# Kernel optimization log

Measured on AMD Instinct MI355X. Metric: run time of the kernel, lower is better.

Reference implementation:

```python
import jax, jax.numpy as jnp
import numpy as np

B, R, A, L, P = 1024, 512, 196, 2, 4  # batch, rnn_size, att_size, num_layers, num_parallels


def setup_inputs() -> dict:
    key = jax.random.key(0)
    ks = jax.random.split(key, 24)
    s = 0.02
    inp = {
        'x': jax.random.normal(ks[0], (B, R), jnp.float32),
        'att': jax.random.normal(ks[1], (B, A, R), jnp.float32),
        'inputs': jax.random.normal(ks[2], (2 * L, B, R), jnp.float32),
        # first attention block
        'Wa2a': jax.random.normal(ks[3], (A, R), jnp.float32) * s,
        'ba2a': jnp.zeros((A,), jnp.float32),
        'Wh2a': jax.random.normal(ks[4], (A, R), jnp.float32) * s,
        'bh2a': jnp.zeros((A,), jnp.float32),
        'Wd2d': jax.random.normal(ks[5], (1, A), jnp.float32) * s,
        'bd2d': jnp.zeros((1,), jnp.float32),
        # second attention block
        'Wa2a1': jax.random.normal(ks[6], (A, R), jnp.float32) * s,
        'ba2a1': jnp.zeros((A,), jnp.float32),
        'Wh2a1': jax.random.normal(ks[7], (A, R), jnp.float32) * s,
        'bh2a1': jnp.zeros((A,), jnp.float32),
        'Wd2d1': jax.random.normal(ks[8], (1, A), jnp.float32) * s,
        'bd2d1': jnp.zeros((1,), jnp.float32),
        # per-parallel LSTM gate linears, stacked over P
        'Wi2h': jax.random.normal(ks[9], (P, 4 * R, R), jnp.float32) * s,
        'bi2h': jnp.zeros((P, 4 * R), jnp.float32),
        'Wh2h': jax.random.normal(ks[10], (P, 4 * R, R), jnp.float32) * s,
        'bh2h': jnp.zeros((P, 4 * R), jnp.float32),
        'Wa2h': jax.random.normal(ks[11], (P, 4 * R, R), jnp.float32) * s,
        'ba2h': jnp.zeros((P, 4 * R), jnp.float32),
    }
    return inp


def _attend(att, h, Wa, ba, Wh, bh, Wd, bd):
    # att: [B, S, R] with S == A (code requires it); h: [B, R]
    av = jnp.einsum('bsr,ar->bsa', att, Wa) + ba            # [B, S, A]
    ah = h @ Wh.T + bh                                      # [B, A]
    # original expands h-projection along the LAST axis (unsqueeze(2).expand)
    dot = jnp.tanh(av + ah[:, :, None])                     # [B, S, A]
    score = jnp.einsum('bsa,a->bs', dot, Wd[0]) + bd[0]     # [B, S]
    w = jax.nn.softmax(score, axis=-1)
    return jnp.einsum('bsr,bs->br', att, w)                 # [B, R]


def reference(x, att, inputs, Wa2a, ba2a, Wh2a, bh2a, Wd2d, bd2d,
              Wa2a1, ba2a1, Wh2a1, bh2a1, Wd2d1, bd2d1,
              Wi2h, bi2h, Wh2h, bh2h, Wa2h, ba2h):
    R_ = x.shape[-1]
    L_ = inputs.shape[0] // 2
    outputs = []
    for i in range(L_):
        prev_c = inputs[2 * i]
        prev_h = inputs[2 * i + 1]
        xt = x if i == 0 else x + outputs[-1]
        att_res = _attend(att, prev_h, Wa2a, ba2a, Wh2a, bh2a, Wd2d, bd2d)
        # stacked per-parallel gate sums: [P, B, 4R]
        sums = (jnp.einsum('bd,pgd->pbg', xt, Wi2h) + bi2h[:, None, :]
                + jnp.einsum('bd,pgd->pbg', prev_h, Wh2h) + bh2h[:, None, :]
                + jnp.einsum('bd,pgd->pbg', att_res, Wa2h) + ba2h[:, None, :])
        ig = jax.nn.sigmoid(sums[..., :R_])
        fg = jax.nn.sigmoid(sums[..., R_:2 * R_])
        og = jax.nn.sigmoid(sums[..., 2 * R_:3 * R_])
        it = jnp.tanh(sums[..., 3 * R_:])
        nc = fg * prev_c[None] + ig * it                    # [P, B, R]
        next_c = nc.mean(axis=0)
        next_h = (og * jnp.tanh(nc)).mean(axis=0)
        att_res1 = _attend(att, next_h, Wa2a1, ba2a1, Wh2a1, bh2a1, Wd2d1, bd2d1)
        top_h = att_res1 + next_h
        outputs.append(next_c)
        outputs.append(top_h)
    return jnp.stack(outputs)  # [2L, B, R]
```

## Files before the change

kernel.cpp:

```cpp
#include <hip/hip_runtime.h>
#include <math.h>

typedef __attribute__((ext_vector_type(8))) unsigned short ushort8_t;
typedef __attribute__((ext_vector_type(8))) short bf16x8;
typedef __attribute__((ext_vector_type(4))) float f32x4;

namespace {

constexpr int Bn = 1024;
constexpr int Rn = 512;
constexpr int An = 196;
constexpr int Gn = 8192;
constexpr int Kcat = 1536;
constexpr int NP = 224;
constexpr long ROWS = (long)Bn * An;

__device__ __forceinline__ float b2f(unsigned short u) {
  union { unsigned int i; float f; } v; v.i = ((unsigned int)u) << 16; return v.f;
}
__device__ __forceinline__ unsigned short f2b(float f) {
  union { float f; unsigned int i; } v; v.f = f;
  unsigned int r = v.i + 0x7fffu + ((v.i >> 16) & 1u);
  return (unsigned short)(r >> 16);
}
__device__ __forceinline__ float sigmf(float x) {
  return __builtin_amdgcn_rcpf(1.f + __expf(-x));
}
__device__ __forceinline__ float tanhf_fast(float x) {
  const float e = __expf(2.f * x);
  return 1.f - 2.f * __builtin_amdgcn_rcpf(e + 1.f);
}

__global__ __launch_bounds__(256)
void f2b_copy(const float* __restrict__ src, unsigned short* __restrict__ dst, long n)
{
  long i = ((long)blockIdx.x * 256 + threadIdx.x) * 8;
  const long stride = (long)gridDim.x * 256 * 8;
  for (; i + 8 <= n; i += stride) {
    float4 a = *(const float4*)(src + i);
    float4 b = *(const float4*)(src + i + 4);
    ushort8_t o;
    o[0] = f2b(a.x); o[1] = f2b(a.y); o[2] = f2b(a.z); o[3] = f2b(a.w);
    o[4] = f2b(b.x); o[5] = f2b(b.y); o[6] = f2b(b.z); o[7] = f2b(b.w);
    *(ushort8_t*)(dst + i) = o;
  }
}

__global__ __launch_bounds__(256)
void pack_wpad(const float* __restrict__ Wa0, const float* __restrict__ Wa1,
               unsigned short* __restrict__ Wp)
{
  long i = ((long)blockIdx.x * 256 + threadIdx.x) * 8;
  if (i >= 2L * NP * 512) return;
  const int set = (int)(i / (NP * 512));
  const int rem = (int)(i % (NP * 512));
  const int row = rem / 512, k = rem % 512;
  ushort8_t o;
  if (row < An) {
    const float* s = (set ? Wa1 : Wa0) + (long)row * 512 + k;
    float4 a = *(const float4*)s, b = *(const float4*)(s + 4);
    o[0] = f2b(a.x); o[1] = f2b(a.y); o[2] = f2b(a.z); o[3] = f2b(a.w);
    o[4] = f2b(b.x); o[5] = f2b(b.y); o[6] = f2b(b.z); o[7] = f2b(b.w);
  } else {
    o = ushort8_t{0,0,0,0,0,0,0,0};
  }
  *(ushort8_t*)(Wp + i) = o;
}

__global__ __launch_bounds__(256)
void pack_w(const float* __restrict__ Wi, const float* __restrict__ Wh,
            const float* __restrict__ Wa, unsigned short* __restrict__ W2)
{
  long i = ((long)blockIdx.x * 256 + threadIdx.x) * 8;
  if (i >= (long)Gn * Kcat) return;
  const int g = (int)(i / Kcat);
  const int k = (int)(i % Kcat);
  const float* src = (k < 512) ? Wi + (long)g * 512 + k
                   : (k < 1024) ? Wh + (long)g * 512 + (k - 512)
                   : Wa + (long)g * 512 + (k - 1024);
  float4 a = *(const float4*)src;
  float4 b = *(const float4*)(src + 4);
  ushort8_t o;
  o[0] = f2b(a.x); o[1] = f2b(a.y); o[2] = f2b(a.z); o[3] = f2b(a.w);
  o[4] = f2b(b.x); o[5] = f2b(b.y); o[6] = f2b(b.z); o[7] = f2b(b.w);
  *(ushort8_t*)(W2 + i) = o;
}

__global__ __launch_bounds__(256)
void pack_x(const float* __restrict__ xa, const float* __restrict__ xb,
            const float* __restrict__ h, const float* __restrict__ a,
            unsigned short* __restrict__ X2)
{
  long i = ((long)blockIdx.x * 256 + threadIdx.x) * 8;
  if (i >= (long)Bn * Kcat) return;
  const int b = (int)(i / Kcat);
  const int k = (int)(i % Kcat);
  ushort8_t o;
  if (k < 512) {
    const float* s = xa + (long)b * 512 + k;
    float4 v0 = *(const float4*)s, v1 = *(const float4*)(s + 4);
    if (xb) {
      const float* s2 = xb + (long)b * 512 + k;
      float4 w0 = *(const float4*)s2, w1 = *(const float4*)(s2 + 4);
      v0.x += w0.x; v0.y += w0.y; v0.z += w0.z; v0.w += w0.w;
      v1.x += w1.x; v1.y += w1.y; v1.z += w1.z; v1.w += w1.w;
    }
    o[0] = f2b(v0.x); o[1] = f2b(v0.y); o[2] = f2b(v0.z); o[3] = f2b(v0.w);
    o[4] = f2b(v1.x); o[5] = f2b(v1.y); o[6] = f2b(v1.z); o[7] = f2b(v1.w);
  } else {
    const float* s = (k < 1024) ? h + (long)b * 512 + (k - 512)
                                : a + (long)b * 512 + (k - 1024);
    float4 v0 = *(const float4*)s, v1 = *(const float4*)(s + 4);
    o[0] = f2b(v0.x); o[1] = f2b(v0.y); o[2] = f2b(v0.z); o[3] = f2b(v0.w);
    o[4] = f2b(v1.x); o[5] = f2b(v1.y); o[6] = f2b(v1.z); o[7] = f2b(v1.w);
  }
  *(ushort8_t*)(X2 + i) = o;
}

__global__ __launch_bounds__(512)
void av_all(const float* __restrict__ A32,
            unsigned short* __restrict__ att_out,
            const unsigned short* __restrict__ Wcat,
            const float* __restrict__ b0vec, const float* __restrict__ b1vec,
            const float* __restrict__ Wd,
            const float* __restrict__ ah0, const float* __restrict__ ah1,
            float* __restrict__ s0, float* __restrict__ s1,
            unsigned short* __restrict__ av_out)
{
  constexpr int LDP = 40;
  __shared__ unsigned short As[128 * LDP];
  __shared__ unsigned short Bs[448 * LDP];
  __shared__ float wds[NP], bas0[NP], bas1[NP];
  __shared__ float ahAs[128], ahBs[128];
  __shared__ float sbA[128], sbB[128];

  const int tid = threadIdx.x;
  const int lane = tid & 63, wid = tid >> 6;
  const int wr = wid >> 2, wc = wid & 3;
  const int fr = lane & 15, q = lane >> 4, kg = q * 8;
  const long row0 = (long)blockIdx.x * 128;

  if (tid < NP) {
    bas0[tid] = (tid < An) ? b0vec[tid] : 0.f;
    bas1[tid] = (tid < An) ? b1vec[tid] : 0.f;
    wds[tid]  = (tid < An) ? Wd[tid] : 0.f;
  }
  if (tid >= 256 && tid < 384) {
    ahAs[tid - 256] = ah0[row0 + tid - 256];
    ahBs[tid - 256] = ah1[row0 + tid - 256];
  }

  f32x4 acc[4][7] = {};

  const int arow = tid >> 2, akc = (tid & 3) * 8;
  const float* Ap = A32 + (row0 + arow) * 512 + akc;
  unsigned short* Aout = att_out + (row0 + arow) * 512 + akc;
  const bool bload = tid < 448;
  const unsigned short* Bp = Wcat + (long)tid * 512;

  float4 fa0 = *(const float4*)Ap;
  float4 fa1 = *(const float4*)(Ap + 4);
  ushort8_t pb0{}, pb1{}, pb2{}, pb3{};
  if (bload) {
    pb0 = *(const ushort8_t*)(Bp);
    pb1 = *(const ushort8_t*)(Bp + 8);
    pb2 = *(const ushort8_t*)(Bp + 16);
    pb3 = *(const ushort8_t*)(Bp + 24);
  }
  const int swA = arow * LDP + akc;
  const int swB = tid * LDP;

  for (int kt = 0; kt < 512; kt += 32) {
    ushort8_t ua;
    ua[0] = f2b(fa0.x); ua[1] = f2b(fa0.y); ua[2] = f2b(fa0.z); ua[3] = f2b(fa0.w);
    ua[4] = f2b(fa1.x); ua[5] = f2b(fa1.y); ua[6] = f2b(fa1.z); ua[7] = f2b(fa1.w);
    *(ushort8_t*)&As[swA] = ua;
    *(ushort8_t*)(Aout + kt) = ua;
    if (bload) {
      *(ushort8_t*)&Bs[swB] = pb0;
      *(ushort8_t*)&Bs[swB + 8] = pb1;
      *(ushort8_t*)&Bs[swB + 16] = pb2;
      *(ushort8_t*)&Bs[swB + 24] = pb3;
    }
    if (kt + 32 < 512) {
      fa0 = *(const float4*)(Ap + kt + 32);
      fa1 = *(const float4*)(Ap + kt + 36);
      if (bload) {
        pb0 = *(const ushort8_t*)(Bp + kt + 32);
        pb1 = *(const ushort8_t*)(Bp + kt + 40);
        pb2 = *(const ushort8_t*)(Bp + kt + 48);
        pb3 = *(const ushort8_t*)(Bp + kt + 56);
      }
    }
    __syncthreads();
    bf16x8 af[4], bfr[7];
#pragma unroll
    for (int m = 0; m < 4; ++m)
      af[m] = *(const bf16x8*)&As[(wr * 64 + m * 16 + fr) * LDP + kg];
#pragma unroll
    for (int n = 0; n < 7; ++n)
      bfr[n] = *(const bf16x8*)&Bs[(wc * 112 + n * 16 + fr) * LDP + kg];
#pragma unroll
    for (int m = 0; m < 4; ++m)
#pragma unroll
      for (int n = 0; n < 7; ++n)
        acc[m][n] = __builtin_amdgcn_mfma_f32_16x16x32_bf16(af[m], bfr[n], acc[m][n], 0, 0, 0);
    __syncthreads();
  }

  float pA[4][4], pB[4][4];
#pragma unroll
  for (int m = 0; m < 4; ++m)
#pragma unroll
    for (int j = 0; j < 4; ++j) { pA[m][j] = 0.f; pB[m][j] = 0.f; }

  if (wc < 2) {
#pragma unroll
    for (int n = 0; n < 7; ++n) {
      const int col = wc * 112 + n * 16 + fr;
      const float wd = wds[col];
      const float bv = bas0[col];
#pragma unroll
      for (int m = 0; m < 4; ++m) {
#pragma unroll
        for (int j = 0; j < 4; ++j) {
          const int rl = wr * 64 + m * 16 + q * 4 + j;
          const float av = acc[m][n][j] + bv;
          pA[m][j] += wd * tanhf_fast(av + ahAs[rl]);
          pB[m][j] += wd * tanhf_fast(av + ahBs[rl]);
        }
      }
    }
#pragma unroll
    for (int m = 0; m < 4; ++m)
#pragma unroll
      for (int j = 0; j < 4; ++j) {
#pragma unroll
        for (int off = 1; off < 16; off <<= 1) {
          pA[m][j] += __shfl_xor(pA[m][j], off);
          pB[m][j] += __shfl_xor(pB[m][j], off);
        }
      }
  } else {
#pragma unroll
    for (int n = 0; n < 7; ++n) {
      const int col1 = (wc - 2) * 112 + n * 16 + fr;
      if (col1 >= An) continue;
      const float bv = bas1[col1];
#pragma unroll
      for (int m = 0; m < 4; ++m) {
#pragma unroll
        for (int j = 0; j < 4; ++j) {
          const long row = row0 + wr * 64 + m * 16 + q * 4 + j;
          av_out[row * An + col1] = f2b(acc[m][n][j] + bv);
        }
      }
    }
  }
  __syncthreads();
  if (wc == 0 && fr == 0) {
#pragma unroll
    for (int m = 0; m < 4; ++m)
#pragma unroll
      for (int j = 0; j < 4; ++j) {
        const int rl = wr * 64 + m * 16 + q * 4 + j;
        sbA[rl] = pA[m][j]; sbB[rl] = pB[m][j];
      }
  }
  __syncthreads();
  if (wc == 1 && fr == 0) {
#pragma unroll
    for (int m = 0; m < 4; ++m)
#pragma unroll
      for (int j = 0; j < 4; ++j) {
        const int rl = wr * 64 + m * 16 + q * 4 + j;
        sbA[rl] += pA[m][j]; sbB[rl] += pB[m][j];
      }
  }
  __syncthreads();
  if (tid < 128) {
    s0[row0 + tid] = sbA[tid];
    s1[row0 + tid] = sbB[tid];
  }
}

__global__ __launch_bounds__(256)
void gemm_bf(const unsigned short* __restrict__ A, const unsigned short* __restrict__ Bm,
             const float* __restrict__ bias, float* __restrict__ C,
             int N, int K, int ldc)
{
  constexpr int LDP = 40;
  __shared__ unsigned short As[128 * LDP];
  __shared__ unsigned short Bs[128 * LDP];
  const int tid = threadIdx.x;
  const long row0 = (long)blockIdx.y * 128;
  const int col0 = blockIdx.x * 128;
  const int wid = tid >> 6, lane = tid & 63;
  const int wr = wid >> 1, wc = wid & 1;
  const int fr = lane & 15, kg = (lane >> 4) * 8;

  f32x4 acc[4][4] = {};

  const int srow = tid >> 1;
  const int skh = tid & 1;
  const unsigned short* Ap = A + (row0 + srow) * (long)K + skh * 16;
  const int bcol = col0 + srow;
  const unsigned short* Bp = Bm + (long)(bcol < N ? bcol : N - 1) * K + skh * 16;

  ushort8_t a0 = *(const ushort8_t*)(Ap);
  ushort8_t a1 = *(const ushort8_t*)(Ap + 8);
  ushort8_t b0 = *(const ushort8_t*)(Bp);
  ushort8_t b1 = *(const ushort8_t*)(Bp + 8);

  const int sw = srow * LDP + skh * 16;
  for (int kt = 0; kt < K; kt += 32) {
    *(ushort8_t*)&As[sw] = a0;
    *(ushort8_t*)&As[sw + 8] = a1;
    *(ushort8_t*)&Bs[sw] = b0;
    *(ushort8_t*)&Bs[sw + 8] = b1;
    if (kt + 32 < K) {
      a0 = *(const ushort8_t*)(Ap + kt + 32);
      a1 = *(const ushort8_t*)(Ap + kt + 40);
      b0 = *(const ushort8_t*)(Bp + kt + 32);
      b1 = *(const ushort8_t*)(Bp + kt + 40);
    }
    __syncthreads();
    bf16x8 af[4], bfr[4];
#pragma unroll
    for (int m = 0; m < 4; ++m)
      af[m] = *(const bf16x8*)&As[(wr * 64 + m * 16 + fr) * LDP + kg];
#pragma unroll
    for (int n = 0; n < 4; ++n)
      bfr[n] = *(const bf16x8*)&Bs[(wc * 64 + n * 16 + fr) * LDP + kg];
#pragma unroll
    for (int m = 0; m < 4; ++m)
#pragma unroll
      for (int n = 0; n < 4; ++n)
        acc[m][n] = __builtin_amdgcn_mfma_f32_16x16x32_bf16(af[m], bfr[n], acc[m][n], 0, 0, 0);
    __syncthreads();
  }

  const int crow = wr * 64 + (lane >> 4) * 4;
  const int ccol = wc * 64 + fr;
#pragma unroll
  for (int n = 0; n < 4; ++n) {
    const int col = col0 + ccol + n * 16;
    if (col >= N) continue;
    const float bv = bias ? bias[col] : 0.f;
#pragma unroll
    for (int m = 0; m < 4; ++m) {
      const long rb = row0 + crow + m * 16;
#pragma unroll
      for (int j = 0; j < 4; ++j)
        C[(rb + j) * (long)ldc + col] = acc[m][n][j] + bv;
    }
  }
}

__global__ __launch_bounds__(256)
void score1(const unsigned short* __restrict__ av, const float* __restrict__ ah,
            const float* __restrict__ Wd, float* __restrict__ s0)
{
  const int row = blockIdx.x * 4 + (threadIdx.x >> 6);
  const int lane = threadIdx.x & 63;
  const unsigned short* avp = av + (long)row * An;
  const float A0 = ah[row];
  float v0 = 0.f;
  for (int a = lane; a < An; a += 64)
    v0 += Wd[a] * tanhf_fast(b2f(avp[a]) + A0);
#pragma unroll
  for (int o = 32; o; o >>= 1) v0 += __shfl_down(v0, o);
  if (lane == 0) s0[row] = v0;
}

__global__ __launch_bounds__(256)
void softmax_rows(float* __restrict__ sc)
{
  const int b = blockIdx.x;
  const int t = threadIdx.x;
  float x = (t < An) ? sc[(long)b * An + t] : -3.0e38f;
  float m = x;
#pragma unroll
  for (int o = 32; o > 0; o >>= 1) m = fmaxf(m, __shfl_down(m, o));
  __shared__ float red[4];
  __shared__ float bmax, bsumv;
  const int wid = t >> 6;
  if ((t & 63) == 0) red[wid] = m;
  __syncthreads();
  if (t == 0) bmax = fmaxf(fmaxf(red[0], red[1]), fmaxf(red[2], red[3]));
  __syncthreads();
  float e = (t < An) ? __expf(x - bmax) : 0.f;
  float sm = e;
#pragma unroll
  for (int o = 32; o > 0; o >>= 1) sm += __shfl_down(sm, o);
  if ((t & 63) == 0) red[wid] = sm;
  __syncthreads();
  if (t == 0) bsumv = red[0] + red[1] + red[2] + red[3];
  __syncthreads();
  if (t < An) sc[(long)b * An + t] = e / bsumv;
}

template<bool DUAL>
__global__ __launch_bounds__(256)
void wsum2(const unsigned short* __restrict__ att,
           const float* __restrict__ w0, const float* __restrict__ w1,
           const float* __restrict__ add0,
           float* __restrict__ o0, float* __restrict__ o1)
{
  const int half = threadIdx.x >> 7;
  const int b = blockIdx.x * 2 + half;
  const int t = threadIdx.x & 127;
  __shared__ float ws0[2][An], ws1[2][An];
  for (int s = t; s < An; s += 128) {
    ws0[half][s] = w0[(long)b * An + s];
    if (DUAL) ws1[half][s] = w1[(long)b * An + s];
  }
  __syncthreads();
  const unsigned short* ap = att + (long)b * An * Rn + t * 4;
  float a00 = 0, a01 = 0, a02 = 0, a03 = 0;
  float a10 = 0, a11 = 0, a12 = 0, a13 = 0;
  for (int s = 0; s < An; ++s) {
    ushort4 u = *(const ushort4*)(ap + (long)s * Rn);
    const float f0 = b2f(u.x), f1 = b2f(u.y), f2 = b2f(u.z), f3 = b2f(u.w);
    const float v0 = ws0[half][s];
    a00 = fmaf(f0, v0, a00); a01 = fmaf(f1, v0, a01);
    a02 = fmaf(f2, v0, a02); a03 = fmaf(f3, v0, a03);
    if (DUAL) {
      const float v1 = ws1[half][s];
      a10 = fmaf(f0, v1, a10); a11 = fmaf(f1, v1, a11);
      a12 = fmaf(f2, v1, a12); a13 = fmaf(f3, v1, a13);
    }
  }
  const long base = (long)b * Rn + t * 4;
  if (add0) {
    float4 ad = *(const float4*)(add0 + base);
    a00 += ad.x; a01 += ad.y; a02 += ad.z; a03 += ad.w;
  }
  float4 r0 = make_float4(a00, a01, a02, a03);
  *(float4*)(o0 + base) = r0;
  if (DUAL) *(float4*)(o1 + base) = make_float4(a10, a11, a12, a13);
}

__global__ __launch_bounds__(256)
void gates_pw(const float* __restrict__ sums, const float* __restrict__ prev_c,
              float* __restrict__ out_c, float* __restrict__ nh,
              unsigned short* __restrict__ nh_bf)
{
  const int i = blockIdx.x * 256 + threadIdx.x;
  const int b = i >> 9;
  const int r = i & 511;
  const float c = prev_c[i];
  float aC = 0.f, aH = 0.f;
#pragma unroll
  for (int p = 0; p < 4; ++p) {
    const float* sp = sums + (long)b * Gn + p * 2048 + r;
    const float ig = sigmf(sp[0]);
    const float fg = sigmf(sp[512]);
    const float og = sigmf(sp[1024]);
    const float it = tanhf_fast(sp[1536]);
    const float nc = fmaf(fg, c, ig * it);
    aC += nc;
    aH = fmaf(og, tanhf_fast(nc), aH);
  }
  out_c[i] = aC * 0.25f;
  const float hv = aH * 0.25f;
  nh[i] = hv;
  nh_bf[i] = f2b(hv);
}

__global__ __launch_bounds__(256)
void bias3(const float* __restrict__ a, const float* __restrict__ b,
           const float* __restrict__ c, float* __restrict__ o, int n)
{
  const int i = blockIdx.x * 256 + threadIdx.x;
  if (i < n) o[i] = a[i] + b[i] + c[i];
}

}

extern "C" void kernel_launch(void* const* d_in, const int* in_sizes, int n_in,
                              void* d_out, int out_size, void* d_ws, size_t ws_size,
                              hipStream_t stream)
{
  const float* x      = (const float*)d_in[0];
  const float* att    = (const float*)d_in[1];
  const float* inputs = (const float*)d_in[2];
  const float* Wa2a   = (const float*)d_in[3];
  const float* ba2a   = (const float*)d_in[4];
  const float* Wh2a   = (const float*)d_in[5];
  const float* bh2a   = (const float*)d_in[6];
  const float* Wd2d   = (const float*)d_in[7];
  const float* Wa2a1  = (const float*)d_in[9];
  const float* ba2a1  = (const float*)d_in[10];
  const float* Wh2a1  = (const float*)d_in[11];
  const float* bh2a1  = (const float*)d_in[12];
  const float* Wd2d1  = (const float*)d_in[13];
  const float* Wi2h   = (const float*)d_in[15];
  const float* bi2h   = (const float*)d_in[16];
  const float* Wh2h   = (const float*)d_in[17];
  const float* bh2h   = (const float*)d_in[18];
  const float* Wa2h   = (const float*)d_in[19];
  const float* ba2h   = (const float*)d_in[20];
  (void)in_sizes; (void)n_in; (void)out_size; (void)ws_size;

  float* out = (float*)d_out;
  const float* prev_c0 = inputs + 0 * (long)Bn * Rn;
  const float* prev_h0 = inputs + 1 * (long)Bn * Rn;
  const float* prev_c1 = inputs + 2 * (long)Bn * Rn;
  const float* prev_h1 = inputs + 3 * (long)Bn * Rn;

  char* wsp = (char*)d_ws;
  size_t off = 0;
  auto alloc = [&](size_t bytes) -> void* {
    void* p = wsp + off;
    off += (bytes + 1023) & ~(size_t)1023;
    return p;
  };
  unsigned short* att_bf  = (unsigned short*)alloc(ROWS * Rn * 2);
  unsigned short* W2      = (unsigned short*)alloc((size_t)Gn * Kcat * 2);
  unsigned short* Wpad    = (unsigned short*)alloc((size_t)2 * NP * Rn * 2);
  unsigned short* wh2a_bf = (unsigned short*)alloc((size_t)An * Rn * 2);
  unsigned short* wh2a1_bf= (unsigned short*)alloc((size_t)An * Rn * 2);
  unsigned short* h0_bf   = (unsigned short*)alloc((size_t)Bn * Rn * 2);
  unsigned short* h1_bf   = (unsigned short*)alloc((size_t)Bn * Rn * 2);
  unsigned short* nh_bf   = (unsigned short*)alloc((size_t)Bn * Rn * 2);
  unsigned short* X2      = (unsigned short*)alloc((size_t)Bn * Kcat * 2);
  unsigned short* av1_bf  = (unsigned short*)alloc(ROWS * An * 2);
  float* ahA  = (float*)alloc(ROWS * 4);
  float* ahB  = (float*)alloc(ROWS * 4);
  float* ah1  = (float*)alloc(ROWS * 4);
  float* scA  = (float*)alloc(ROWS * 4);
  float* scB  = (float*)alloc(ROWS * 4);
  float* sc1  = (float*)alloc(ROWS * 4);
  float* res0 = (float*)alloc((size_t)Bn * Rn * 4);
  float* res1 = (float*)alloc((size_t)Bn * Rn * 4);
  float* nh   = (float*)alloc((size_t)Bn * Rn * 4);
  float* bsum = (float*)alloc((size_t)Gn * 4);
  float* sums = (float*)alloc((size_t)Bn * Gn * 4);

  const dim3 blk(256);

  pack_wpad<<<dim3(112), blk, 0, stream>>>(Wa2a, Wa2a1, Wpad);
  f2b_copy<<<dim3(49), blk, 0, stream>>>(Wh2a,  wh2a_bf,  (long)An * Rn);
  f2b_copy<<<dim3(49), blk, 0, stream>>>(Wh2a1, wh2a1_bf, (long)An * Rn);
  f2b_copy<<<dim3(256), blk, 0, stream>>>(prev_h0, h0_bf, (long)Bn * Rn);
  f2b_copy<<<dim3(256), blk, 0, stream>>>(prev_h1, h1_bf, (long)Bn * Rn);
  pack_w<<<dim3(6144), blk, 0, stream>>>(Wi2h, Wh2h, Wa2h, W2);
  bias3<<<dim3(Gn / 256), blk, 0, stream>>>(bi2h, bh2h, ba2h, bsum, Gn);

  gemm_bf<<<dim3(2, Bn / 128), blk, 0, stream>>>(h0_bf, wh2a_bf, bh2a, ahA, An, Rn, An);
  gemm_bf<<<dim3(2, Bn / 128), blk, 0, stream>>>(h1_bf, wh2a_bf, bh2a, ahB, An, Rn, An);

  av_all<<<dim3((int)(ROWS / 128)), dim3(512), 0, stream>>>(
      att, att_bf, Wpad, ba2a, ba2a1, Wd2d, ahA, ahB, scA, scB, av1_bf);
  softmax_rows<<<dim3(Bn), blk, 0, stream>>>(scA);
  softmax_rows<<<dim3(Bn), blk, 0, stream>>>(scB);
  wsum2<true><<<dim3(Bn / 2), blk, 0, stream>>>(att_bf, scA, scB, (const float*)nullptr, res0, res1);

  pack_x<<<dim3(768), blk, 0, stream>>>(x, (const float*)nullptr, prev_h0, res0, X2);
  gemm_bf<<<dim3(Gn / 128, Bn / 128), blk, 0, stream>>>(X2, W2, bsum, sums, Gn, Kcat, Gn);
  gates_pw<<<dim3(Bn * Rn / 256), blk, 0, stream>>>(sums, prev_c0, out + 0, nh, nh_bf);

  gemm_bf<<<dim3(2, Bn / 128), blk, 0, stream>>>(nh_bf, wh2a1_bf, bh2a1, ah1, An, Rn, An);
  score1<<<dim3((int)(ROWS / 4)), blk, 0, stream>>>(av1_bf, ah1, Wd2d1, sc1);
  softmax_rows<<<dim3(Bn), blk, 0, stream>>>(sc1);
  wsum2<false><<<dim3(Bn / 2), blk, 0, stream>>>(att_bf, sc1, (const float*)nullptr, nh,
                                                 out + (long)Bn * Rn, (float*)nullptr);

  pack_x<<<dim3(768), blk, 0, stream>>>(x, out + (long)Bn * Rn, prev_h1, res1, X2);
  gemm_bf<<<dim3(Gn / 128, Bn / 128), blk, 0, stream>>>(X2, W2, bsum, sums, Gn, Kcat, Gn);
  gates_pw<<<dim3(Bn * Rn / 256), blk, 0, stream>>>(sums, prev_c1, out + 2 * (long)Bn * Rn, nh, nh_bf);

  gemm_bf<<<dim3(2, Bn / 128), blk, 0, stream>>>(nh_bf, wh2a1_bf, bh2a1, ah1, An, Rn, An);
  score1<<<dim3((int)(ROWS / 4)), blk, 0, stream>>>(av1_bf, ah1, Wd2d1, sc1);
  softmax_rows<<<dim3(Bn), blk, 0, stream>>>(sc1);
  wsum2<false><<<dim3(Bn / 2), blk, 0, stream>>>(att_bf, sc1, (const float*)nullptr, nh,
                                                 out + 3 * (long)Bn * Rn, (float*)nullptr);
}
```

Before: 737.4 us.

## Fuse softmax into weighted sum, add direct-to-LDS gate GEMM, pre-convert att

Removes the separate softmax_rows launches and computes the row softmax inside wsum2 before the weighted sum. Adds a dedicated gate GEMM that uses global_load_lds direct-to-LDS loads and a swizzled block order in place of the generic gemm_bf. The att fp32-to-bf16 conversion moves out of the attention GEMM into a standalone f2b_copy pass. LDS padding grows from 40 to 56. The standalone conversion adds an extra full pass over att, and the new gate GEMM has no padding or double buffering, so LDS bank conflicts and exposed load latency are possible.

```diff
diff --git a/kernel.cpp b/kernel.cpp
--- a/kernel.cpp
+++ b/kernel.cpp
@@ -118,16 +118,15 @@
 }
 
 __global__ __launch_bounds__(512)
-void av_all(const float* __restrict__ A32,
-            unsigned short* __restrict__ att_out,
-            const unsigned short* __restrict__ Wcat,
-            const float* __restrict__ b0vec, const float* __restrict__ b1vec,
-            const float* __restrict__ Wd,
-            const float* __restrict__ ah0, const float* __restrict__ ah1,
-            float* __restrict__ s0, float* __restrict__ s1,
-            unsigned short* __restrict__ av_out)
-{
-  constexpr int LDP = 40;
+void av_both(const unsigned short* __restrict__ A,
+             const unsigned short* __restrict__ Wcat,
+             const float* __restrict__ b0vec, const float* __restrict__ b1vec,
+             const float* __restrict__ Wd,
+             const float* __restrict__ ah0, const float* __restrict__ ah1,
+             float* __restrict__ s0, float* __restrict__ s1,
+             unsigned short* __restrict__ av_out)
+{
+  constexpr int LDP = 56;
   __shared__ unsigned short As[128 * LDP];
   __shared__ unsigned short Bs[448 * LDP];
   __shared__ float wds[NP], bas0[NP], bas1[NP];
@@ -153,13 +152,11 @@
   f32x4 acc[4][7] = {};
 
   const int arow = tid >> 2, akc = (tid & 3) * 8;
-  const float* Ap = A32 + (row0 + arow) * 512 + akc;
-  unsigned short* Aout = att_out + (row0 + arow) * 512 + akc;
+  const unsigned short* Ap = A + (row0 + arow) * 512 + akc;
   const bool bload = tid < 448;
   const unsigned short* Bp = Wcat + (long)tid * 512;
 
-  float4 fa0 = *(const float4*)Ap;
-  float4 fa1 = *(const float4*)(Ap + 4);
+  ushort8_t pa = *(const ushort8_t*)Ap;
   ushort8_t pb0{}, pb1{}, pb2{}, pb3{};
   if (bload) {
     pb0 = *(const ushort8_t*)(Bp);
@@ -171,11 +168,7 @@
   const int swB = tid * LDP;
 
   for (int kt = 0; kt < 512; kt += 32) {
-    ushort8_t ua;
-    ua[0] = f2b(fa0.x); ua[1] = f2b(fa0.y); ua[2] = f2b(fa0.z); ua[3] = f2b(fa0.w);
-    ua[4] = f2b(fa1.x); ua[5] = f2b(fa1.y); ua[6] = f2b(fa1.z); ua[7] = f2b(fa1.w);
-    *(ushort8_t*)&As[swA] = ua;
-    *(ushort8_t*)(Aout + kt) = ua;
+    *(ushort8_t*)&As[swA] = pa;
     if (bload) {
       *(ushort8_t*)&Bs[swB] = pb0;
       *(ushort8_t*)&Bs[swB + 8] = pb1;
@@ -183,8 +176,7 @@
       *(ushort8_t*)&Bs[swB + 24] = pb3;
     }
     if (kt + 32 < 512) {
-      fa0 = *(const float4*)(Ap + kt + 32);
-      fa1 = *(const float4*)(Ap + kt + 36);
+      pa = *(const ushort8_t*)(Ap + kt + 32);
       if (bload) {
         pb0 = *(const ushort8_t*)(Bp + kt + 32);
         pb1 = *(const ushort8_t*)(Bp + kt + 40);
@@ -285,11 +277,78 @@
 }
 
 __global__ __launch_bounds__(256)
+void gemm_gate(const unsigned short* __restrict__ A, const unsigned short* __restrict__ Bm,
+               const float* __restrict__ bias, float* __restrict__ C)
+{
+  __shared__ unsigned short As[128 * 32];
+  __shared__ unsigned short Bs[128 * 32];
+  const int tid = threadIdx.x;
+  const int lane = tid & 63, w = tid >> 6;
+  int bid = blockIdx.x;
+  bid = (bid & 7) * (gridDim.x >> 3) + (bid >> 3);
+  const int bx = bid & 63;
+  const int by = bid >> 6;
+  const long row0 = (long)by * 128;
+  const long col0 = (long)bx * 128;
+  const int wr = w >> 1, wc = w & 1;
+  const int fr = lane & 15, q = lane >> 4;
+  const int srow = lane >> 2, schk = lane & 3;
+
+  f32x4 acc[4][4] = {};
+  const unsigned short* A0 = A + row0 * Kcat + schk * 8;
+  const unsigned short* B0 = Bm + col0 * Kcat + schk * 8;
+
+  for (int kt = 0; kt < Kcat; kt += 32) {
+#pragma unroll
+    for (int i = 0; i < 2; ++i) {
+      const int rr = (w * 2 + i) * 16 + srow;
+      __builtin_amdgcn_global_load_lds(
+          (const __attribute__((address_space(1))) unsigned int*)(A0 + (long)rr * Kcat + kt),
+          (__attribute__((address_space(3))) unsigned int*)(As + (w * 2 + i) * 512),
+          16, 0, 0);
+      __builtin_amdgcn_global_load_lds(
+          (const __attribute__((address_space(1))) unsigned int*)(B0 + (long)rr * Kcat + kt),
+          (__attribute__((address_space(3))) unsigned int*)(Bs + (w * 2 + i) * 512),
+          16, 0, 0);
+    }
+    __syncthreads();
+    bf16x8 af[4], bfr[4];
+#pragma unroll
+    for (int m = 0; m < 4; ++m)
+      af[m] = *(const bf16x8*)&As[(wr * 64 + m * 16 + fr) * 32 + q * 8];
+#pragma unroll
+    for (int n = 0; n < 4; ++n)
+      bfr[n] = *(const bf16x8*)&Bs[(wc * 64 + n * 16 + fr) * 32 + q * 8];
+#pragma unroll
+    for (int m = 0; m < 4; ++m)
+#pragma unroll
+      for (int n = 0; n < 4; ++n)
+        acc[m][n] = __builtin_amdgcn_mfma_f32_16x16x32_bf16(af[m], bfr[n], acc[m][n], 0, 0, 0);
+    __syncthreads();
+  }
+
+  const int crow = wr * 64 + q * 4;
+  const int ccol = wc * 64 + fr;
+#pragma unroll
+  for (int n = 0; n < 4; ++n) {
+    const int col = (int)col0 + ccol + n * 16;
+    const float bv = bias[col];
+#pragma unroll
+    for (int m = 0; m < 4; ++m) {
+      const long rb = row0 + crow + m * 16;
+#pragma unroll
+      for (int j = 0; j < 4; ++j)
+        C[(rb + j) * (long)Gn + col] = acc[m][n][j] + bv;
+    }
+  }
+}
+
+__global__ __launch_bounds__(256)
 void gemm_bf(const unsigned short* __restrict__ A, const unsigned short* __restrict__ Bm,
              const float* __restrict__ bias, float* __restrict__ C,
              int N, int K, int ldc)
 {
-  constexpr int LDP = 40;
+  constexpr int LDP = 56;
   __shared__ unsigned short As[128 * LDP];
   __shared__ unsigned short Bs[128 * LDP];
   const int tid = threadIdx.x;
@@ -373,33 +432,6 @@
   if (lane == 0) s0[row] = v0;
 }
 
-__global__ __launch_bounds__(256)
-void softmax_rows(float* __restrict__ sc)
-{
-  const int b = blockIdx.x;
-  const int t = threadIdx.x;
-  float x = (t < An) ? sc[(long)b * An + t] : -3.0e38f;
-  float m = x;
-#pragma unroll
-  for (int o = 32; o > 0; o >>= 1) m = fmaxf(m, __shfl_down(m, o));
-  __shared__ float red[4];
-  __shared__ float bmax, bsumv;
-  const int wid = t >> 6;
-  if ((t & 63) == 0) red[wid] = m;
-  __syncthreads();
-  if (t == 0) bmax = fmaxf(fmaxf(red[0], red[1]), fmaxf(red[2], red[3]));
-  __syncthreads();
-  float e = (t < An) ? __expf(x - bmax) : 0.f;
-  float sm = e;
-#pragma unroll
-  for (int o = 32; o > 0; o >>= 1) sm += __shfl_down(sm, o);
-  if ((t & 63) == 0) red[wid] = sm;
-  __syncthreads();
-  if (t == 0) bsumv = red[0] + red[1] + red[2] + red[3];
-  __syncthreads();
-  if (t < An) sc[(long)b * An + t] = e / bsumv;
-}
-
 template<bool DUAL>
 __global__ __launch_bounds__(256)
 void wsum2(const unsigned short* __restrict__ att,
@@ -410,12 +442,53 @@
   const int half = threadIdx.x >> 7;
   const int b = blockIdx.x * 2 + half;
   const int t = threadIdx.x & 127;
+  const int wv = t >> 6;
   __shared__ float ws0[2][An], ws1[2][An];
-  for (int s = t; s < An; s += 128) {
-    ws0[half][s] = w0[(long)b * An + s];
-    if (DUAL) ws1[half][s] = w1[(long)b * An + s];
-  }
+  __shared__ float redm[2][2][2], redsum[2][2][2];
+
+  const float r0a = w0[(long)b * An + t];
+  const float r0b = (t + 128 < An) ? w0[(long)b * An + t + 128] : -3.0e38f;
+  float r1a = -3.0e38f, r1b = -3.0e38f;
+  if (DUAL) {
+    r1a = w1[(long)b * An + t];
+    r1b = (t + 128 < An) ? w1[(long)b * An + t + 128] : -3.0e38f;
+  }
+  float m0 = fmaxf(r0a, r0b), m1 = fmaxf(r1a, r1b);
+#pragma unroll
+  for (int o = 32; o; o >>= 1) {
+    m0 = fmaxf(m0, __shfl_xor(m0, o));
+    if (DUAL) m1 = fmaxf(m1, __shfl_xor(m1, o));
+  }
+  if ((t & 63) == 0) { redm[0][half][wv] = m0; if (DUAL) redm[1][half][wv] = m1; }
   __syncthreads();
+  m0 = fmaxf(redm[0][half][0], redm[0][half][1]);
+  if (DUAL) m1 = fmaxf(redm[1][half][0], redm[1][half][1]);
+  const float e0a = __expf(r0a - m0);
+  const float e0b = (t + 128 < An) ? __expf(r0b - m0) : 0.f;
+  float sl0 = e0a + e0b, sl1 = 0.f;
+  float e1a = 0.f, e1b = 0.f;
+  if (DUAL) {
+    e1a = __expf(r1a - m1);
+    e1b = (t + 128 < An) ? __expf(r1b - m1) : 0.f;
+    sl1 = e1a + e1b;
+  }
+#pragma unroll
+  for (int o = 32; o; o >>= 1) {
+    sl0 += __shfl_xor(sl0, o);
+    if (DUAL) sl1 += __shfl_xor(sl1, o);
+  }
+  if ((t & 63) == 0) { redsum[0][half][wv] = sl0; if (DUAL) redsum[1][half][wv] = sl1; }
+  __syncthreads();
+  const float inv0 = __builtin_amdgcn_rcpf(redsum[0][half][0] + redsum[0][half][1]);
+  ws0[half][t] = e0a * inv0;
+  if (t + 128 < An) ws0[half][t + 128] = e0b * inv0;
+  if (DUAL) {
+    const float inv1 = __builtin_amdgcn_rcpf(redsum[1][half][0] + redsum[1][half][1]);
+    ws1[half][t] = e1a * inv1;
+    if (t + 128 < An) ws1[half][t + 128] = e1b * inv1;
+  }
+  __syncthreads();
+
   const unsigned short* ap = att + (long)b * An * Rn + t * 4;
   float a00 = 0, a01 = 0, a02 = 0, a03 = 0;
   float a10 = 0, a11 = 0, a12 = 0, a13 = 0;
@@ -436,8 +509,7 @@
     float4 ad = *(const float4*)(add0 + base);
     a00 += ad.x; a01 += ad.y; a02 += ad.z; a03 += ad.w;
   }
-  float4 r0 = make_float4(a00, a01, a02, a03);
-  *(float4*)(o0 + base) = r0;
+  *(float4*)(o0 + base) = make_float4(a00, a01, a02, a03);
   if (DUAL) *(float4*)(o1 + base) = make_float4(a10, a11, a12, a13);
 }
 
@@ -540,6 +612,7 @@
 
   const dim3 blk(256);
 
+  f2b_copy<<<dim3(50176), blk, 0, stream>>>(att, att_bf, ROWS * Rn);
   pack_wpad<<<dim3(112), blk, 0, stream>>>(Wa2a, Wa2a1, Wpad);
   f2b_copy<<<dim3(49), blk, 0, stream>>>(Wh2a,  wh2a_bf,  (long)An * Rn);
   f2b_copy<<<dim3(49), blk, 0, stream>>>(Wh2a1, wh2a1_bf, (long)An * Rn);
@@ -551,29 +624,25 @@
   gemm_bf<<<dim3(2, Bn / 128), blk, 0, stream>>>(h0_bf, wh2a_bf, bh2a, ahA, An, Rn, An);
   gemm_bf<<<dim3(2, Bn / 128), blk, 0, stream>>>(h1_bf, wh2a_bf, bh2a, ahB, An, Rn, An);
 
-  av_all<<<dim3((int)(ROWS / 128)), dim3(512), 0, stream>>>(
-      att, att_bf, Wpad, ba2a, ba2a1, Wd2d, ahA, ahB, scA, scB, av1_bf);
-  softmax_rows<<<dim3(Bn), blk, 0, stream>>>(scA);
-  softmax_rows<<<dim3(Bn), blk, 0, stream>>>(scB);
+  av_both<<<dim3((int)(ROWS / 128)), dim3(512), 0, stream>>>(
+      att_bf, Wpad, ba2a, ba2a1, Wd2d, ahA, ahB, scA, scB, av1_bf);
   wsum2<true><<<dim3(Bn / 2), blk, 0, stream>>>(att_bf, scA, scB, (const float*)nullptr, res0, res1);
 
   pack_x<<<dim3(768), blk, 0, stream>>>(x, (const float*)nullptr, prev_h0, res0, X2);
-  gemm_bf<<<dim3(Gn / 128, Bn / 128), blk, 0, stream>>>(X2, W2, bsum, sums, Gn, Kcat, Gn);
+  gemm_gate<<<dim3(512), blk, 0, stream>>>(X2, W2, bsum, sums);
   gates_pw<<<dim3(Bn * Rn / 256), blk, 0, stream>>>(sums, prev_c0, out + 0, nh, nh_bf);
 
   gemm_bf<<<dim3(2, Bn / 128), blk, 0, stream>>>(nh_bf, wh2a1_bf, bh2a1, ah1, An, Rn, An);
   score1<<<dim3((int)(ROWS / 4)), blk, 0, stream>>>(av1_bf, ah1, Wd2d1, sc1);
-  softmax_rows<<<dim3(Bn), blk, 0, stream>>>(sc1);
   wsum2<false><<<dim3(Bn / 2), blk, 0, stream>>>(att_bf, sc1, (const float*)nullptr, nh,
                                                  out + (long)Bn * Rn, (float*)nullptr);
 
   pack_x<<<dim3(768), blk, 0, stream>>>(x, out + (long)Bn * Rn, prev_h1, res1, X2);
-  gemm_bf<<<dim3(Gn / 128, Bn / 128), blk, 0, stream>>>(X2, W2, bsum, sums, Gn, Kcat, Gn);
+  gemm_gate<<<dim3(512), blk, 0, stream>>>(X2, W2, bsum, sums);
   gates_pw<<<dim3(Bn * Rn / 256), blk, 0, stream>>>(sums, prev_c1, out + 2 * (long)Bn * Rn, nh, nh_bf);
 
   gemm_bf<<<dim3(2, Bn / 128), blk, 0, stream>>>(nh_bf, wh2a1_bf, bh2a1, ah1, An, Rn, An);
   score1<<<dim3((int)(ROWS / 4)), blk, 0, stream>>>(av1_bf, ah1, Wd2d1, sc1);
-  softmax_rows<<<dim3(Bn), blk, 0, stream>>>(sc1);
   wsum2<false><<<dim3(Bn / 2), blk, 0, stream>>>(att_bf, sc1, (const float*)nullptr, nh,
                                                  out + 3 * (long)Bn * Rn, (float*)nullptr);
 }
```

Result: slower. 765.7 us (+3.8%).
